# Kernel optimization log

Measured on AMD Instinct MI355X. Metric: run time of the kernel, lower is better.

The kernel has to match this reference:

```python
import jax, jax.numpy as jnp
import numpy as np

NUM_BINS = 256


def _equalize_channel(chan):
    # chan: (P,) int32 pixel values in [0, 255]. PIL/torchvision-style equalize.
    hist = jnp.zeros(NUM_BINS, jnp.float32).at[chan].add(1.0)
    total = hist.sum()
    # value of the last nonzero histogram bin (excluded from step computation)
    nz = hist > 0
    last_idx = (NUM_BINS - 1) - jnp.argmax(nz[::-1])
    last = hist[last_idx]
    step = jnp.floor((total - last) / 255.0)
    cum = jnpp_cumsum = jnp.cumsum(hist)
    lut = jnp.floor((cum + jnp.floor(step / 2.0)) / jnp.maximum(step, 1.0))
    # shift right by one (pad a leading 0, drop last) and clamp to [0,255]
    lut = jnp.clip(jnp.concatenate([jnp.zeros(1, jnp.float32), lut[:-1]]), 0.0, 255.0)
    ident = jnp.arange(NUM_BINS, dtype=jnp.float32)
    lut = jnp.where(step == 0, ident, lut)  # step==0 -> identity mapping
    return lut[chan]


def _equalize(x):
    # x: (N, C, H, W) float, pixel values -> uint8 semantics
    N, C, H, W = x.shape
    xi = jnp.clip(x, 0, 255).astype(jnp.int32).reshape(N * C, H * W)
    out = jax.vmap(_equalize_channel)(xi)  # (N*C, H*W) float32
    return out.reshape(N, C, H, W).astype(x.dtype)


def setup_inputs() -> dict:
    key = jax.random.key(0)
    x = jax.random.uniform(key, (64, 3, 512, 512), dtype=jnp.float32) * 255.0
    magnitude = 5
    return {"x": x, "magnitude": magnitude}


def reference(x, magnitude):
    # magnitude is unused in the original forward (Equalize ignores it)
    return _equalize(x)
```

## Files before the change

### kernel.cpp

```cpp
#include <hip/hip_runtime.h>

#define NBINS 256
#define NCHAN 192
#define HIST_BPC 8
#define APPLY_BPC 8
#define TPB 256
#define VEC_PER_CHAN (512 * 512 / 4)
#define NCOPY 16

typedef float f4 __attribute__((ext_vector_type(4)));

__global__ __launch_bounds__(TPB) void hist_kernel(const float* __restrict__ x,
                                                   int* __restrict__ partials) {
    __shared__ int lh[NBINS * NCOPY];
    const int chan = blockIdx.x / HIST_BPC;
    const int blk  = blockIdx.x % HIST_BPC;
    const int tid  = threadIdx.x;
    const int cp   = (tid & 63) >> 2;

    for (int i = tid; i < NBINS * NCOPY; i += TPB) lh[i] = 0;
    __syncthreads();

    const int vecPerBlock = VEC_PER_CHAN / HIST_BPC;
    const size_t base = (size_t)chan * VEC_PER_CHAN + (size_t)blk * vecPerBlock;
    const f4* bx = (const f4*)x + base;

    #pragma unroll 4
    for (int i = tid; i < vecPerBlock; i += TPB) {
        f4 v = bx[i];
        int a = (int)fminf(fmaxf(v.x, 0.f), 255.f);
        int b = (int)fminf(fmaxf(v.y, 0.f), 255.f);
        int c = (int)fminf(fmaxf(v.z, 0.f), 255.f);
        int d = (int)fminf(fmaxf(v.w, 0.f), 255.f);
        atomicAdd(&lh[(a << 4) + cp], 1);
        atomicAdd(&lh[(b << 4) + cp], 1);
        atomicAdd(&lh[(c << 4) + cp], 1);
        atomicAdd(&lh[(d << 4) + cp], 1);
    }
    __syncthreads();

    int s = 0;
    #pragma unroll
    for (int k = 0; k < NCOPY; ++k) s += lh[(tid << 4) + ((tid + k) & 15)];
    partials[(chan * HIST_BPC + blk) * NBINS + tid] = s;
}

__global__ __launch_bounds__(TPB) void lut_kernel(const int* __restrict__ partials,
                                                  float* __restrict__ lut) {
    __shared__ int scan[NBINS];
    __shared__ int s_last_idx, s_last;
    const int chan = blockIdx.x;
    const int tid  = threadIdx.x;

    int h = 0;
    #pragma unroll
    for (int b = 0; b < HIST_BPC; ++b)
        h += partials[(chan * HIST_BPC + b) * NBINS + tid];
    scan[tid] = h;
    if (tid == 0) s_last_idx = 0;
    __syncthreads();
    if (h > 0) atomicMax(&s_last_idx, tid);

    for (int off = 1; off < NBINS; off <<= 1) {
        __syncthreads();
        int t = (tid >= off) ? scan[tid - off] : 0;
        __syncthreads();
        scan[tid] += t;
    }
    __syncthreads();
    if (tid == s_last_idx) s_last = h;
    __syncthreads();

    const int total = scan[NBINS - 1];
    const int step  = (total - s_last) / 255;

    float lutv;
    if (step == 0)      lutv = (float)tid;
    else if (tid == 0)  lutv = 0.f;
    else {
        int l = (scan[tid - 1] + (step >> 1)) / step;
        lutv = (float)(l < 255 ? l : 255);
    }
    lut[chan * NBINS + tid] = lutv;
}

__global__ __launch_bounds__(TPB) void apply_kernel(const float* __restrict__ x,
                                                    float* __restrict__ out,
                                                    const float* __restrict__ lut) {
    __shared__ float slut[NBINS * NCOPY];
    const int chan = blockIdx.x / APPLY_BPC;
    const int blk  = blockIdx.x % APPLY_BPC;
    const int tid  = threadIdx.x;
    const int cp   = (tid & 63) >> 2;

    const float lv = lut[chan * NBINS + tid];
    #pragma unroll
    for (int k = 0; k < NCOPY; ++k) slut[(tid << 4) + ((tid + k) & 15)] = lv;
    __syncthreads();

    const int vecPerBlock = VEC_PER_CHAN / APPLY_BPC;
    const size_t base = (size_t)chan * VEC_PER_CHAN + (size_t)blk * vecPerBlock;
    const f4* bx = (const f4*)x + base;
    f4* bo = (f4*)out + base;

    #pragma unroll 4
    for (int i = tid; i < vecPerBlock; i += TPB) {
        f4 v = bx[i];
        int a = (int)fminf(fmaxf(v.x, 0.f), 255.f);
        int b = (int)fminf(fmaxf(v.y, 0.f), 255.f);
        int c = (int)fminf(fmaxf(v.z, 0.f), 255.f);
        int d = (int)fminf(fmaxf(v.w, 0.f), 255.f);
        f4 o;
        o.x = slut[(a << 4) + cp];
        o.y = slut[(b << 4) + cp];
        o.z = slut[(c << 4) + cp];
        o.w = slut[(d << 4) + cp];
        __builtin_nontemporal_store(o, &bo[i]);
    }
}

extern "C" void kernel_launch(void* const* d_in, const int* in_sizes, int n_in,
                              void* d_out, int out_size, void* d_ws, size_t ws_size,
                              hipStream_t stream) {
    const float* x = (const float*)d_in[0];
    float* out = (float*)d_out;

    int* partials = (int*)d_ws;
    float* lut = (float*)((int*)d_ws + (size_t)NCHAN * HIST_BPC * NBINS);

    hist_kernel<<<NCHAN * HIST_BPC, TPB, 0, stream>>>(x, partials);
    lut_kernel<<<NCHAN, TPB, 0, stream>>>(partials, lut);
    apply_kernel<<<NCHAN * APPLY_BPC, TPB, 0, stream>>>(x, out, lut);
}
```

Before: 370.9 us.

## Fuse histogram, LUT and apply into one block-per-channel kernel

Replaces the three-kernel pipeline (partial histograms, LUT scan, LUT apply) with a single kernel in which one 1024-thread block handles a whole channel. It builds the histogram in LDS with 32 replicated copies, does the scan and LUT build in place, then remaps pixels with a replicated LUT. This removes two launches and the workspace round-trip for partial histograms and LUTs. In exchange, only 192 blocks run, fewer than the number of CUs, so per-CU LDS atomic throughput and memory parallelism may limit performance. Each block also rereads its 1 MB channel after the histogram phase.

```diff
diff --git a/kernel.cpp b/kernel.cpp
--- a/kernel.cpp
+++ b/kernel.cpp
@@ -2,119 +2,92 @@
 
 #define NBINS 256
 #define NCHAN 192
-#define HIST_BPC 8
-#define APPLY_BPC 8
-#define TPB 256
-#define VEC_PER_CHAN (512 * 512 / 4)
-#define NCOPY 16
+#define TPB 1024
+#define VEC_PER_CHAN 65536
+#define NCOPY 32
 
 typedef float f4 __attribute__((ext_vector_type(4)));
 
-__global__ __launch_bounds__(TPB) void hist_kernel(const float* __restrict__ x,
-                                                   int* __restrict__ partials) {
-    __shared__ int lh[NBINS * NCOPY];
-    const int chan = blockIdx.x / HIST_BPC;
-    const int blk  = blockIdx.x % HIST_BPC;
+__global__ __launch_bounds__(TPB) void equalize_fused(const float* __restrict__ x,
+                                                      float* __restrict__ out) {
+    __shared__ int   lh[NBINS * NCOPY];
+    __shared__ float slut[NBINS * NCOPY];
+    __shared__ int   scan[NBINS];
+    __shared__ int   s_last_idx, s_last;
+
+    const int chan = blockIdx.x;
     const int tid  = threadIdx.x;
-    const int cp   = (tid & 63) >> 2;
+    const int cp   = (tid & 63) >> 1;
 
     for (int i = tid; i < NBINS * NCOPY; i += TPB) lh[i] = 0;
+    if (tid == 0) s_last_idx = 0;
     __syncthreads();
 
-    const int vecPerBlock = VEC_PER_CHAN / HIST_BPC;
-    const size_t base = (size_t)chan * VEC_PER_CHAN + (size_t)blk * vecPerBlock;
+    const size_t base = (size_t)chan * VEC_PER_CHAN;
     const f4* bx = (const f4*)x + base;
 
     #pragma unroll 4
-    for (int i = tid; i < vecPerBlock; i += TPB) {
+    for (int i = tid; i < VEC_PER_CHAN; i += TPB) {
         f4 v = bx[i];
         int a = (int)fminf(fmaxf(v.x, 0.f), 255.f);
         int b = (int)fminf(fmaxf(v.y, 0.f), 255.f);
         int c = (int)fminf(fmaxf(v.z, 0.f), 255.f);
         int d = (int)fminf(fmaxf(v.w, 0.f), 255.f);
-        atomicAdd(&lh[(a << 4) + cp], 1);
-        atomicAdd(&lh[(b << 4) + cp], 1);
-        atomicAdd(&lh[(c << 4) + cp], 1);
-        atomicAdd(&lh[(d << 4) + cp], 1);
+        atomicAdd(&lh[(a << 5) + cp], 1);
+        atomicAdd(&lh[(b << 5) + cp], 1);
+        atomicAdd(&lh[(c << 5) + cp], 1);
+        atomicAdd(&lh[(d << 5) + cp], 1);
     }
     __syncthreads();
 
-    int s = 0;
-    #pragma unroll
-    for (int k = 0; k < NCOPY; ++k) s += lh[(tid << 4) + ((tid + k) & 15)];
-    partials[(chan * HIST_BPC + blk) * NBINS + tid] = s;
-}
-
-__global__ __launch_bounds__(TPB) void lut_kernel(const int* __restrict__ partials,
-                                                  float* __restrict__ lut) {
-    __shared__ int scan[NBINS];
-    __shared__ int s_last_idx, s_last;
-    const int chan = blockIdx.x;
-    const int tid  = threadIdx.x;
-
     int h = 0;
-    #pragma unroll
-    for (int b = 0; b < HIST_BPC; ++b)
-        h += partials[(chan * HIST_BPC + b) * NBINS + tid];
-    scan[tid] = h;
-    if (tid == 0) s_last_idx = 0;
+    if (tid < NBINS) {
+        #pragma unroll
+        for (int k = 0; k < NCOPY; ++k) h += lh[(tid << 5) + ((tid + k) & 31)];
+        scan[tid] = h;
+    }
     __syncthreads();
-    if (h > 0) atomicMax(&s_last_idx, tid);
+    if (tid < NBINS && h > 0) atomicMax(&s_last_idx, tid);
 
     for (int off = 1; off < NBINS; off <<= 1) {
+        int t = 0;
+        if (tid >= off && tid < NBINS) t = scan[tid - off];
         __syncthreads();
-        int t = (tid >= off) ? scan[tid - off] : 0;
+        if (tid < NBINS) scan[tid] += t;
         __syncthreads();
-        scan[tid] += t;
     }
-    __syncthreads();
     if (tid == s_last_idx) s_last = h;
     __syncthreads();
 
     const int total = scan[NBINS - 1];
     const int step  = (total - s_last) / 255;
 
-    float lutv;
-    if (step == 0)      lutv = (float)tid;
-    else if (tid == 0)  lutv = 0.f;
-    else {
-        int l = (scan[tid - 1] + (step >> 1)) / step;
-        lutv = (float)(l < 255 ? l : 255);
+    if (tid < NBINS) {
+        float lutv;
+        if (step == 0)      lutv = (float)tid;
+        else if (tid == 0)  lutv = 0.f;
+        else {
+            int l = (scan[tid - 1] + (step >> 1)) / step;
+            lutv = (float)(l < 255 ? l : 255);
+        }
+        #pragma unroll
+        for (int k = 0; k < NCOPY; ++k) slut[(tid << 5) + ((tid + k) & 31)] = lutv;
     }
-    lut[chan * NBINS + tid] = lutv;
-}
-
-__global__ __launch_bounds__(TPB) void apply_kernel(const float* __restrict__ x,
-                                                    float* __restrict__ out,
-                                                    const float* __restrict__ lut) {
-    __shared__ float slut[NBINS * NCOPY];
-    const int chan = blockIdx.x / APPLY_BPC;
-    const int blk  = blockIdx.x % APPLY_BPC;
-    const int tid  = threadIdx.x;
-    const int cp   = (tid & 63) >> 2;
-
-    const float lv = lut[chan * NBINS + tid];
-    #pragma unroll
-    for (int k = 0; k < NCOPY; ++k) slut[(tid << 4) + ((tid + k) & 15)] = lv;
     __syncthreads();
 
-    const int vecPerBlock = VEC_PER_CHAN / APPLY_BPC;
-    const size_t base = (size_t)chan * VEC_PER_CHAN + (size_t)blk * vecPerBlock;
-    const f4* bx = (const f4*)x + base;
     f4* bo = (f4*)out + base;
-
     #pragma unroll 4
-    for (int i = tid; i < vecPerBlock; i += TPB) {
+    for (int i = tid; i < VEC_PER_CHAN; i += TPB) {
         f4 v = bx[i];
         int a = (int)fminf(fmaxf(v.x, 0.f), 255.f);
         int b = (int)fminf(fmaxf(v.y, 0.f), 255.f);
         int c = (int)fminf(fmaxf(v.z, 0.f), 255.f);
         int d = (int)fminf(fmaxf(v.w, 0.f), 255.f);
         f4 o;
-        o.x = slut[(a << 4) + cp];
-        o.y = slut[(b << 4) + cp];
-        o.z = slut[(c << 4) + cp];
-        o.w = slut[(d << 4) + cp];
+        o.x = slut[(a << 5) + cp];
+        o.y = slut[(b << 5) + cp];
+        o.z = slut[(c << 5) + cp];
+        o.w = slut[(d << 5) + cp];
         __builtin_nontemporal_store(o, &bo[i]);
     }
 }
@@ -124,11 +97,7 @@
                               hipStream_t stream) {
     const float* x = (const float*)d_in[0];
     float* out = (float*)d_out;
+    (void)d_ws; (void)ws_size;
 
-    int* partials = (int*)d_ws;
-    float* lut = (float*)((int*)d_ws + (size_t)NCHAN * HIST_BPC * NBINS);
-
-    hist_kernel<<<NCHAN * HIST_BPC, TPB, 0, stream>>>(x, partials);
-    lut_kernel<<<NCHAN, TPB, 0, stream>>>(partials, lut);
-    apply_kernel<<<NCHAN * APPLY_BPC, TPB, 0, stream>>>(x, out, lut);
+    equalize_fused<<<NCHAN, TPB, 0, stream>>>(x, out);
 }
```

After: 365.5 us. About the same (-1.4%).

## Fuse histogram, LUT and apply into one cooperative kernel with grid sync

Applied to the files above, without the earlier changes.

Replaces the three-kernel pipeline with a single cooperative kernel. It builds per-block partial histograms, runs a grid-wide sync, and then has every apply block compute its channel's LUT redundantly before remapping pixels. If the cooperative launch fails it falls back to two kernels that still compute the LUT inside the apply kernel. This removes a kernel launch and the separate LUT pass, and a block may re-read its slice while it is still in L2/MALL. The cost is a grid barrier, redundant scans per block, and the requirement that all 1536 blocks be co-resident.

```diff
diff --git a/kernel.cpp b/kernel.cpp
--- a/kernel.cpp
+++ b/kernel.cpp
@@ -1,32 +1,31 @@
 #include <hip/hip_runtime.h>
+#include <hip/hip_cooperative_groups.h>
+
+namespace cg = cooperative_groups;
 
 #define NBINS 256
 #define NCHAN 192
-#define HIST_BPC 8
-#define APPLY_BPC 8
+#define BPC 8
 #define TPB 256
-#define VEC_PER_CHAN (512 * 512 / 4)
 #define NCOPY 16
+#define VPB 8192
 
 typedef float f4 __attribute__((ext_vector_type(4)));
 
-__global__ __launch_bounds__(TPB) void hist_kernel(const float* __restrict__ x,
-                                                   int* __restrict__ partials) {
-    __shared__ int lh[NBINS * NCOPY];
-    const int chan = blockIdx.x / HIST_BPC;
-    const int blk  = blockIdx.x % HIST_BPC;
-    const int tid  = threadIdx.x;
-    const int cp   = (tid & 63) >> 2;
+__device__ __forceinline__ void phaseA_hist(const float* __restrict__ x,
+                                            int* __restrict__ partials,
+                                            int* lh) {
+    const int tid = threadIdx.x;
+    const int cp  = (tid & 63) >> 2;
 
     for (int i = tid; i < NBINS * NCOPY; i += TPB) lh[i] = 0;
     __syncthreads();
 
-    const int vecPerBlock = VEC_PER_CHAN / HIST_BPC;
-    const size_t base = (size_t)chan * VEC_PER_CHAN + (size_t)blk * vecPerBlock;
+    const size_t base = (size_t)blockIdx.x * VPB;
     const f4* bx = (const f4*)x + base;
 
     #pragma unroll 4
-    for (int i = tid; i < vecPerBlock; i += TPB) {
+    for (int i = tid; i < VPB; i += TPB) {
         f4 v = bx[i];
         int a = (int)fminf(fmaxf(v.x, 0.f), 255.f);
         int b = (int)fminf(fmaxf(v.y, 0.f), 255.f);
@@ -42,37 +41,38 @@
     int s = 0;
     #pragma unroll
     for (int k = 0; k < NCOPY; ++k) s += lh[(tid << 4) + ((tid + k) & 15)];
-    partials[(chan * HIST_BPC + blk) * NBINS + tid] = s;
+    partials[blockIdx.x * NBINS + tid] = s;
 }
 
-__global__ __launch_bounds__(TPB) void lut_kernel(const int* __restrict__ partials,
-                                                  float* __restrict__ lut) {
-    __shared__ int scan[NBINS];
-    __shared__ int s_last_idx, s_last;
-    const int chan = blockIdx.x;
+__device__ __forceinline__ void phaseBC_apply(const float* __restrict__ x,
+                                              float* __restrict__ out,
+                                              const int* __restrict__ partials,
+                                              int* lh, int* scan,
+                                              int* s_last_idx, int* s_last) {
+    const int chan = blockIdx.x / BPC;
     const int tid  = threadIdx.x;
+    const int cp   = (tid & 63) >> 2;
 
     int h = 0;
     #pragma unroll
-    for (int b = 0; b < HIST_BPC; ++b)
-        h += partials[(chan * HIST_BPC + b) * NBINS + tid];
+    for (int b = 0; b < BPC; ++b)
+        h += partials[(chan * BPC + b) * NBINS + tid];
     scan[tid] = h;
-    if (tid == 0) s_last_idx = 0;
+    if (tid == 0) *s_last_idx = 0;
     __syncthreads();
-    if (h > 0) atomicMax(&s_last_idx, tid);
+    if (h > 0) atomicMax(s_last_idx, tid);
 
     for (int off = 1; off < NBINS; off <<= 1) {
-        __syncthreads();
         int t = (tid >= off) ? scan[tid - off] : 0;
         __syncthreads();
         scan[tid] += t;
+        __syncthreads();
     }
-    __syncthreads();
-    if (tid == s_last_idx) s_last = h;
+    if (tid == *s_last_idx) *s_last = h;
     __syncthreads();
 
     const int total = scan[NBINS - 1];
-    const int step  = (total - s_last) / 255;
+    const int step  = (total - *s_last) / 255;
 
     float lutv;
     if (step == 0)      lutv = (float)tid;
@@ -81,30 +81,17 @@
         int l = (scan[tid - 1] + (step >> 1)) / step;
         lutv = (float)(l < 255 ? l : 255);
     }
-    lut[chan * NBINS + tid] = lutv;
-}
-
-__global__ __launch_bounds__(TPB) void apply_kernel(const float* __restrict__ x,
-                                                    float* __restrict__ out,
-                                                    const float* __restrict__ lut) {
-    __shared__ float slut[NBINS * NCOPY];
-    const int chan = blockIdx.x / APPLY_BPC;
-    const int blk  = blockIdx.x % APPLY_BPC;
-    const int tid  = threadIdx.x;
-    const int cp   = (tid & 63) >> 2;
-
-    const float lv = lut[chan * NBINS + tid];
+    float* slut = (float*)lh;
     #pragma unroll
-    for (int k = 0; k < NCOPY; ++k) slut[(tid << 4) + ((tid + k) & 15)] = lv;
+    for (int k = 0; k < NCOPY; ++k) slut[(tid << 4) + ((tid + k) & 15)] = lutv;
     __syncthreads();
 
-    const int vecPerBlock = VEC_PER_CHAN / APPLY_BPC;
-    const size_t base = (size_t)chan * VEC_PER_CHAN + (size_t)blk * vecPerBlock;
+    const size_t base = (size_t)blockIdx.x * VPB;
     const f4* bx = (const f4*)x + base;
     f4* bo = (f4*)out + base;
 
     #pragma unroll 4
-    for (int i = tid; i < vecPerBlock; i += TPB) {
+    for (int i = tid; i < VPB; i += TPB) {
         f4 v = bx[i];
         int a = (int)fminf(fmaxf(v.x, 0.f), 255.f);
         int b = (int)fminf(fmaxf(v.y, 0.f), 255.f);
@@ -119,16 +106,44 @@
     }
 }
 
+__global__ __launch_bounds__(TPB) void equalize_coop(const float* __restrict__ x,
+                                                     float* __restrict__ out,
+                                                     int* __restrict__ partials) {
+    __shared__ int lh[NBINS * NCOPY];
+    __shared__ int scan[NBINS];
+    __shared__ int s_last_idx, s_last;
+    phaseA_hist(x, partials, lh);
+    cg::this_grid().sync();
+    phaseBC_apply(x, out, partials, lh, scan, &s_last_idx, &s_last);
+}
+
+__global__ __launch_bounds__(TPB) void eq_hist(const float* __restrict__ x,
+                                               int* __restrict__ partials) {
+    __shared__ int lh[NBINS * NCOPY];
+    phaseA_hist(x, partials, lh);
+}
+__global__ __launch_bounds__(TPB) void eq_apply(const float* __restrict__ x,
+                                                float* __restrict__ out,
+                                                const int* __restrict__ partials) {
+    __shared__ int lh[NBINS * NCOPY];
+    __shared__ int scan[NBINS];
+    __shared__ int s_last_idx, s_last;
+    phaseBC_apply(x, out, partials, lh, scan, &s_last_idx, &s_last);
+}
+
 extern "C" void kernel_launch(void* const* d_in, const int* in_sizes, int n_in,
                               void* d_out, int out_size, void* d_ws, size_t ws_size,
                               hipStream_t stream) {
     const float* x = (const float*)d_in[0];
     float* out = (float*)d_out;
+    int* partials = (int*)d_ws;
 
-    int* partials = (int*)d_ws;
-    float* lut = (float*)((int*)d_ws + (size_t)NCHAN * HIST_BPC * NBINS);
-
-    hist_kernel<<<NCHAN * HIST_BPC, TPB, 0, stream>>>(x, partials);
-    lut_kernel<<<NCHAN, TPB, 0, stream>>>(partials, lut);
-    apply_kernel<<<NCHAN * APPLY_BPC, TPB, 0, stream>>>(x, out, lut);
+    void* args[] = {(void*)&x, (void*)&out, (void*)&partials};
+    hipError_t e = hipLaunchCooperativeKernel((const void*)equalize_coop,
+                                              dim3(NCHAN * BPC), dim3(TPB),
+                                              args, 0, stream);
+    if (e != hipSuccess) {
+        eq_hist<<<NCHAN * BPC, TPB, 0, stream>>>(x, partials);
+        eq_apply<<<NCHAN * BPC, TPB, 0, stream>>>(x, out, partials);
+    }
 }
```

New measurement: 521.3 us. +40.6%, slower.

## Pack clamped pixel bytes during histogram pass and read them in apply

Applied to the files above, without the earlier changes.

The histogram kernel now writes each pixel's clamped 8-bit value into a packed uint32 workspace buffer, and the apply kernel reads these packed bytes instead of re-reading and re-clamping the float input. This is meant to cut the second full read of the input to a quarter of its size, at the cost of an extra packed write. Input loads use nontemporal hints, and the scan loop's barriers were reordered. Unroll pragmas were dropped.

```diff
diff --git a/kernel.cpp b/kernel.cpp
--- a/kernel.cpp
+++ b/kernel.cpp
@@ -2,36 +2,36 @@
 
 #define NBINS 256
 #define NCHAN 192
-#define HIST_BPC 8
-#define APPLY_BPC 8
+#define BPC 8
 #define TPB 256
-#define VEC_PER_CHAN (512 * 512 / 4)
 #define NCOPY 16
+#define F4_PER_CHAN 65536
+#define F4_PER_BLK (F4_PER_CHAN / BPC)
 
 typedef float f4 __attribute__((ext_vector_type(4)));
 
-__global__ __launch_bounds__(TPB) void hist_kernel(const float* __restrict__ x,
-                                                   int* __restrict__ partials) {
+
+__global__ __launch_bounds__(TPB) void eq_hist_pack(const float* __restrict__ x,
+                                                    unsigned* __restrict__ packed,
+                                                    int* __restrict__ partials) {
     __shared__ int lh[NBINS * NCOPY];
-    const int chan = blockIdx.x / HIST_BPC;
-    const int blk  = blockIdx.x % HIST_BPC;
-    const int tid  = threadIdx.x;
-    const int cp   = (tid & 63) >> 2;
+    const int tid = threadIdx.x;
+    const int cp  = (tid & 63) >> 2;
 
     for (int i = tid; i < NBINS * NCOPY; i += TPB) lh[i] = 0;
     __syncthreads();
 
-    const int vecPerBlock = VEC_PER_CHAN / HIST_BPC;
-    const size_t base = (size_t)chan * VEC_PER_CHAN + (size_t)blk * vecPerBlock;
+    const size_t base = (size_t)blockIdx.x * F4_PER_BLK;
     const f4* bx = (const f4*)x + base;
+    unsigned* bp = packed + base;
 
-    #pragma unroll 4
-    for (int i = tid; i < vecPerBlock; i += TPB) {
-        f4 v = bx[i];
+    for (int i = tid; i < F4_PER_BLK; i += TPB) {
+        f4 v = __builtin_nontemporal_load(&bx[i]);
         int a = (int)fminf(fmaxf(v.x, 0.f), 255.f);
         int b = (int)fminf(fmaxf(v.y, 0.f), 255.f);
         int c = (int)fminf(fmaxf(v.z, 0.f), 255.f);
         int d = (int)fminf(fmaxf(v.w, 0.f), 255.f);
+        bp[i] = (unsigned)(a | (b << 8) | (c << 16) | (d << 24));
         atomicAdd(&lh[(a << 4) + cp], 1);
         atomicAdd(&lh[(b << 4) + cp], 1);
         atomicAdd(&lh[(c << 4) + cp], 1);
@@ -42,11 +42,11 @@
     int s = 0;
     #pragma unroll
     for (int k = 0; k < NCOPY; ++k) s += lh[(tid << 4) + ((tid + k) & 15)];
-    partials[(chan * HIST_BPC + blk) * NBINS + tid] = s;
+    partials[blockIdx.x * NBINS + tid] = s;
 }
 
-__global__ __launch_bounds__(TPB) void lut_kernel(const int* __restrict__ partials,
-                                                  float* __restrict__ lut) {
+__global__ __launch_bounds__(TPB) void eq_lut(const int* __restrict__ partials,
+                                              float* __restrict__ lut) {
     __shared__ int scan[NBINS];
     __shared__ int s_last_idx, s_last;
     const int chan = blockIdx.x;
@@ -54,20 +54,19 @@
 
     int h = 0;
     #pragma unroll
-    for (int b = 0; b < HIST_BPC; ++b)
-        h += partials[(chan * HIST_BPC + b) * NBINS + tid];
+    for (int b = 0; b < BPC; ++b)
+        h += partials[(chan * BPC + b) * NBINS + tid];
     scan[tid] = h;
     if (tid == 0) s_last_idx = 0;
     __syncthreads();
     if (h > 0) atomicMax(&s_last_idx, tid);
 
     for (int off = 1; off < NBINS; off <<= 1) {
-        __syncthreads();
         int t = (tid >= off) ? scan[tid - off] : 0;
         __syncthreads();
         scan[tid] += t;
+        __syncthreads();
     }
-    __syncthreads();
     if (tid == s_last_idx) s_last = h;
     __syncthreads();
 
@@ -84,12 +83,11 @@
     lut[chan * NBINS + tid] = lutv;
 }
 
-__global__ __launch_bounds__(TPB) void apply_kernel(const float* __restrict__ x,
-                                                    float* __restrict__ out,
-                                                    const float* __restrict__ lut) {
+__global__ __launch_bounds__(TPB) void eq_apply(const unsigned* __restrict__ packed,
+                                                float* __restrict__ out,
+                                                const float* __restrict__ lut) {
     __shared__ float slut[NBINS * NCOPY];
-    const int chan = blockIdx.x / APPLY_BPC;
-    const int blk  = blockIdx.x % APPLY_BPC;
+    const int chan = blockIdx.x / BPC;
     const int tid  = threadIdx.x;
     const int cp   = (tid & 63) >> 2;
 
@@ -98,23 +96,17 @@
     for (int k = 0; k < NCOPY; ++k) slut[(tid << 4) + ((tid + k) & 15)] = lv;
     __syncthreads();
 
-    const int vecPerBlock = VEC_PER_CHAN / APPLY_BPC;
-    const size_t base = (size_t)chan * VEC_PER_CHAN + (size_t)blk * vecPerBlock;
-    const f4* bx = (const f4*)x + base;
+    const size_t base = (size_t)blockIdx.x * F4_PER_BLK;
+    const unsigned* bp = packed + base;
     f4* bo = (f4*)out + base;
 
-    #pragma unroll 4
-    for (int i = tid; i < vecPerBlock; i += TPB) {
-        f4 v = bx[i];
-        int a = (int)fminf(fmaxf(v.x, 0.f), 255.f);
-        int b = (int)fminf(fmaxf(v.y, 0.f), 255.f);
-        int c = (int)fminf(fmaxf(v.z, 0.f), 255.f);
-        int d = (int)fminf(fmaxf(v.w, 0.f), 255.f);
+    for (int i = tid; i < F4_PER_BLK; i += TPB) {
+        unsigned p = bp[i];
         f4 o;
-        o.x = slut[(a << 4) + cp];
-        o.y = slut[(b << 4) + cp];
-        o.z = slut[(c << 4) + cp];
-        o.w = slut[(d << 4) + cp];
+        o.x = slut[(int)((p & 255u) << 4) + cp];
+        o.y = slut[(int)(((p >> 8) & 255u) << 4) + cp];
+        o.z = slut[(int)(((p >> 16) & 255u) << 4) + cp];
+        o.w = slut[(int)((p >> 24) << 4) + cp];
         __builtin_nontemporal_store(o, &bo[i]);
     }
 }
@@ -125,10 +117,11 @@
     const float* x = (const float*)d_in[0];
     float* out = (float*)d_out;
 
-    int* partials = (int*)d_ws;
-    float* lut = (float*)((int*)d_ws + (size_t)NCHAN * HIST_BPC * NBINS);
+    unsigned* packed = (unsigned*)d_ws;
+    int* partials = (int*)d_ws + (size_t)NCHAN * F4_PER_CHAN;
+    float* lut = (float*)(partials + (size_t)NCHAN * BPC * NBINS);
 
-    hist_kernel<<<NCHAN * HIST_BPC, TPB, 0, stream>>>(x, partials);
-    lut_kernel<<<NCHAN, TPB, 0, stream>>>(partials, lut);
-    apply_kernel<<<NCHAN * APPLY_BPC, TPB, 0, stream>>>(x, out, lut);
+    eq_hist_pack<<<NCHAN * BPC, TPB, 0, stream>>>(x, packed, partials);
+    eq_lut<<<NCHAN, TPB, 0, stream>>>(partials, lut);
+    eq_apply<<<NCHAN * BPC, TPB, 0, stream>>>(packed, out, lut);
 }
```

Result: faster. 342.0 us (-7.8%).
